# Kernel optimization log

Hardware: AMD Instinct MI355X
Metric: run time of the kernel (lower is better)

## Reference

```python
import jax, jax.numpy as jnp
import numpy as np

N_NODES = 50000
N_EDGES = 800000
IN_FEATS, H_FEATS, N_CLASSES = 64, 64, 16


def setup_inputs() -> dict:
    key = jax.random.key(0)
    ks = jax.random.split(key, 8)
    x = jax.random.normal(ks[0], (N_NODES, IN_FEATS), dtype=jnp.float32)
    src = jax.random.randint(ks[1], (N_EDGES,), 0, N_NODES, dtype=jnp.int64)
    dst = jax.random.randint(ks[2], (N_EDGES,), 0, N_NODES, dtype=jnp.int64)
    W_self1 = jax.random.normal(ks[3], (IN_FEATS, H_FEATS), dtype=jnp.float32) / np.sqrt(IN_FEATS)
    W_neigh1 = jax.random.normal(ks[4], (IN_FEATS, H_FEATS), dtype=jnp.float32) / np.sqrt(IN_FEATS)
    b1 = jnp.zeros((H_FEATS,), dtype=jnp.float32)
    W_self2 = jax.random.normal(ks[5], (H_FEATS, N_CLASSES), dtype=jnp.float32) / np.sqrt(H_FEATS)
    W_neigh2 = jax.random.normal(ks[6], (H_FEATS, N_CLASSES), dtype=jnp.float32) / np.sqrt(H_FEATS)
    b2 = jnp.zeros((N_CLASSES,), dtype=jnp.float32)
    return {"x": x, "src": src, "dst": dst,
            "W_self1": W_self1, "W_neigh1": W_neigh1, "b1": b1,
            "W_self2": W_self2, "W_neigh2": W_neigh2, "b2": b2}


def _mean_agg(h, src, dst, n_nodes):
    # gather source-node features along edges, sum into destinations, divide by in-degree
    summed = jax.ops.segment_sum(h[src], dst, num_segments=n_nodes)  # [N, d]
    deg = jax.ops.segment_sum(jnp.ones_like(src, dtype=h.dtype), dst, num_segments=n_nodes)
    return summed / jnp.maximum(deg, 1.0)[:, None]  # zero in-degree -> zeros (DGL semantics)


def _sage_layer(h, src, dst, W_self, W_neigh, b):
    h_neigh = _mean_agg(h, src, dst, h.shape[0])
    return h @ W_self + h_neigh @ W_neigh + b


def reference(x, src, dst, W_self1, W_neigh1, b1, W_self2, W_neigh2, b2):
    h = _sage_layer(x, src, dst, W_self1, W_neigh1, b1)
    h = jax.nn.relu(h)
    out = _sage_layer(h, src, dst, W_self2, W_neigh2, b2)
    return out
```

## Files before the change

kernel.cpp:

```cpp
#include <hip/hip_runtime.h>
#include <hip/hip_bf16.h>
#include <cstring>


#define FEATS 64
#define CLS   16
#define EPT   16
#define CAP   5120

typedef unsigned short bf16_t;
typedef float floatx2 __attribute__((ext_vector_type(2)));

__device__ __forceinline__ float bfbits2f(unsigned lo16) {
    unsigned v = lo16 << 16;
    float f;
    __builtin_memcpy(&f, &v, 4);
    return f;
}
__device__ __forceinline__ bf16_t f2bf(float f) {
    unsigned u;
    __builtin_memcpy(&u, &f, 4);
    u = (u + 0x7FFFu + ((u >> 16) & 1u)) >> 16;
    return (bf16_t)u;
}
__device__ __forceinline__ unsigned pack2(float a, float b) {
    return (unsigned)f2bf(a) | ((unsigned)f2bf(b) << 16);
}
__device__ __forceinline__ unsigned pack4_fp8(float a, float b, float c, float d) {
    int q = __builtin_amdgcn_cvt_pk_fp8_f32(a, b, 0, false);
    q = __builtin_amdgcn_cvt_pk_fp8_f32(c, d, q, true);
    return (unsigned)q;
}

__global__ __launch_bounds__(256) void fused_pg_kernel(
    const int* __restrict__ src, const int* __restrict__ dst,
    int* __restrict__ bucket_cnt, int* __restrict__ epart, int E,
    const float* __restrict__ x, const float* __restrict__ Ws,
    const float* __restrict__ Wn, bf16_t* __restrict__ selfo,
    unsigned char* __restrict__ t1, int N, int nbp)
{
    __shared__ float smem[16512];
    int t = threadIdx.x;

    if ((int)blockIdx.x < nbp) {
        int* hist = (int*)smem;
        int* base = hist + 256;
        int e0 = blockIdx.x * (256 * EPT);
        hist[t] = 0;
        __syncthreads();
        int pk[EPT];
        int bk[EPT];
#pragma unroll
        for (int j = 0; j < EPT; ++j) {
            int e = e0 + j * 256 + t;
            if (e < E) {
                int d = dst[e];
                pk[j] = (src[e] << 8) | (d & 255);
                bk[j] = d >> 8;
                atomicAdd(&hist[bk[j]], 1);
            } else bk[j] = -1;
        }
        __syncthreads();
        int c = hist[t];
        if (c) base[t] = atomicAdd(&bucket_cnt[t], c);
        hist[t] = 0;
        __syncthreads();
#pragma unroll
        for (int j = 0; j < EPT; ++j) {
            if (bk[j] >= 0) {
                int r = atomicAdd(&hist[bk[j]], 1);
                epart[bk[j] * CAP + base[bk[j]] + r] = pk[j];
            }
        }
        return;
    }

    float* Wc = smem;
    float* xs = smem + 8192;
    int node0 = ((int)blockIdx.x - nbp) * 128;

    for (int idx = t; idx < 64 * 128; idx += 256) {
        int k = idx >> 7, c = idx & 127;
        Wc[idx] = (c < 64) ? Ws[k * 64 + c] : Wn[k * 64 + (c - 64)];
    }
    for (int idx = t; idx < 128 * 16; idx += 256) {
        int row = idx >> 4, c4 = idx & 15;
        int node = node0 + row;
        float4 v = (node < N) ? ((const float4*)(x + (size_t)node * 64))[c4]
                              : make_float4(0.f, 0.f, 0.f, 0.f);
        float* p = &xs[row * 65 + c4 * 4];
        p[0] = v.x; p[1] = v.y; p[2] = v.z; p[3] = v.w;
    }
    __syncthreads();

    int m = t & 31;
    int g = t >> 5;
    float acc[4][16];
#pragma unroll
    for (int j = 0; j < 4; ++j)
#pragma unroll
        for (int c = 0; c < 16; ++c) acc[j][c] = 0.f;

    for (int k = 0; k < 64; ++k) {
        float w[16];
        const float* wp = &Wc[k * 128 + g * 16];
#pragma unroll
        for (int c = 0; c < 16; ++c) w[c] = wp[c];
        float a0 = xs[m * 65 + k];
        float a1 = xs[(m + 32) * 65 + k];
        float a2 = xs[(m + 64) * 65 + k];
        float a3 = xs[(m + 96) * 65 + k];
#pragma unroll
        for (int c = 0; c < 16; ++c) {
            acc[0][c] += a0 * w[c];
            acc[1][c] += a1 * w[c];
            acc[2][c] += a2 * w[c];
            acc[3][c] += a3 * w[c];
        }
    }
#pragma unroll
    for (int j = 0; j < 4; ++j) {
        int node = node0 + m + 32 * j;
        if (node < N) {
            if (g < 4) {
                bf16_t* dstp = selfo + (size_t)node * 64 + g * 16;
                uint4 p0, p1;
                p0.x = pack2(acc[j][0],  acc[j][1]);  p0.y = pack2(acc[j][2],  acc[j][3]);
                p0.z = pack2(acc[j][4],  acc[j][5]);  p0.w = pack2(acc[j][6],  acc[j][7]);
                p1.x = pack2(acc[j][8],  acc[j][9]);  p1.y = pack2(acc[j][10], acc[j][11]);
                p1.z = pack2(acc[j][12], acc[j][13]); p1.w = pack2(acc[j][14], acc[j][15]);
                *(uint4*)(dstp) = p0;
                *(uint4*)(dstp + 8) = p1;
            } else {
                unsigned char* dstp = t1 + (size_t)node * 64 + (g - 4) * 16;
                uint4 q;
                q.x = pack4_fp8(acc[j][0],  acc[j][1],  acc[j][2],  acc[j][3]);
                q.y = pack4_fp8(acc[j][4],  acc[j][5],  acc[j][6],  acc[j][7]);
                q.z = pack4_fp8(acc[j][8],  acc[j][9],  acc[j][10], acc[j][11]);
                q.w = pack4_fp8(acc[j][12], acc[j][13], acc[j][14], acc[j][15]);
                *(uint4*)(dstp) = q;
            }
        }
    }
}

__global__ __launch_bounds__(256) void buildcsr_kernel(const int* __restrict__ epart,
                                                       const int* __restrict__ bucket_cnt,
                                                       int* __restrict__ row_start,
                                                       unsigned short* __restrict__ deg16,
                                                       int* __restrict__ csr, int N) {
    __shared__ int cnt[256];
    __shared__ int pref[256];
    __shared__ int s[256];
    int t = threadIdx.x;
    int b = blockIdx.x;
    int ebeg = b * CAP;
    int ecnt = bucket_cnt[b];
    cnt[t] = 0;
    __syncthreads();
    for (int e = t; e < ecnt; e += 256)
        atomicAdd(&cnt[epart[ebeg + e] & 255], 1);
    __syncthreads();
    int v = cnt[t];
    s[t] = v;
    __syncthreads();
    for (int off = 1; off < 256; off <<= 1) {
        int u = (t >= off) ? s[t - off] : 0;
        __syncthreads();
        s[t] += u;
        __syncthreads();
    }
    pref[t] = s[t] - v;
    int node = b * 256 + t;
    if (node < N) {
        row_start[node] = ebeg + pref[t];
        deg16[node] = (unsigned short)v;
    }
    cnt[t] = 0;
    __syncthreads();
    for (int e = t; e < ecnt; e += 256) {
        int pk = epart[ebeg + e];
        int ln = pk & 255;
        int r = atomicAdd(&cnt[ln], 1);
        csr[ebeg + pref[ln] + r] = pk >> 8;
    }
}

__global__ __launch_bounds__(256) void gather64_kernel(
    const int* __restrict__ csr, const int* __restrict__ row_start,
    const unsigned short* __restrict__ deg16,
    const unsigned char* __restrict__ t1, const bf16_t* __restrict__ selfo,
    bf16_t* __restrict__ h1, const float* __restrict__ b1, int N)
{
    int wid = (blockIdx.x * 256 + threadIdx.x) >> 6;
    int lane = threadIdx.x & 63;
    int eslot = lane >> 4;
    int cg = lane & 15;
    if (wid >= N) return;
    int beg = row_start[wid];
    int d = deg16[wid];
    float ax = 0.f, ay = 0.f, az = 0.f, aw = 0.f;
    int i = eslot;
    for (; i + 12 < d; i += 16) {
        int s0 = csr[beg + i];
        int s1 = csr[beg + i + 4];
        int s2 = csr[beg + i + 8];
        int s3 = csr[beg + i + 12];
        unsigned r0 = *(const unsigned*)(t1 + (size_t)s0 * 64 + cg * 4);
        unsigned r1 = *(const unsigned*)(t1 + (size_t)s1 * 64 + cg * 4);
        unsigned r2 = *(const unsigned*)(t1 + (size_t)s2 * 64 + cg * 4);
        unsigned r3 = *(const unsigned*)(t1 + (size_t)s3 * 64 + cg * 4);
        floatx2 p0 = __builtin_amdgcn_cvt_pk_f32_fp8((int)r0, false);
        floatx2 q0 = __builtin_amdgcn_cvt_pk_f32_fp8((int)r0, true);
        floatx2 p1 = __builtin_amdgcn_cvt_pk_f32_fp8((int)r1, false);
        floatx2 q1 = __builtin_amdgcn_cvt_pk_f32_fp8((int)r1, true);
        floatx2 p2 = __builtin_amdgcn_cvt_pk_f32_fp8((int)r2, false);
        floatx2 q2 = __builtin_amdgcn_cvt_pk_f32_fp8((int)r2, true);
        floatx2 p3 = __builtin_amdgcn_cvt_pk_f32_fp8((int)r3, false);
        floatx2 q3 = __builtin_amdgcn_cvt_pk_f32_fp8((int)r3, true);
        ax += p0.x + p1.x + p2.x + p3.x;
        ay += p0.y + p1.y + p2.y + p3.y;
        az += q0.x + q1.x + q2.x + q3.x;
        aw += q0.y + q1.y + q2.y + q3.y;
    }
    for (; i < d; i += 4) {
        int s0 = csr[beg + i];
        unsigned r0 = *(const unsigned*)(t1 + (size_t)s0 * 64 + cg * 4);
        floatx2 p0 = __builtin_amdgcn_cvt_pk_f32_fp8((int)r0, false);
        floatx2 q0 = __builtin_amdgcn_cvt_pk_f32_fp8((int)r0, true);
        ax += p0.x; ay += p0.y; az += q0.x; aw += q0.y;
    }
    ax += __shfl_xor(ax, 16); ay += __shfl_xor(ay, 16);
    az += __shfl_xor(az, 16); aw += __shfl_xor(aw, 16);
    ax += __shfl_xor(ax, 32); ay += __shfl_xor(ay, 32);
    az += __shfl_xor(az, 32); aw += __shfl_xor(aw, 32);
    if (eslot == 0) {
        float inv = 1.f / fmaxf((float)d, 1.f);
        size_t o = (size_t)wid * 64 + cg * 4;
        uint2 su = *(const uint2*)(selfo + o);
        float4 bb = *(const float4*)(b1 + cg * 4);
        float rx = fmaxf(bfbits2f(su.x & 0xffff) + ax * inv + bb.x, 0.f);
        float ry = fmaxf(bfbits2f(su.x >> 16)    + ay * inv + bb.y, 0.f);
        float rz = fmaxf(bfbits2f(su.y & 0xffff) + az * inv + bb.z, 0.f);
        float rw = fmaxf(bfbits2f(su.y >> 16)    + aw * inv + bb.w, 0.f);
        uint2 pk;
        pk.x = pack2(rx, ry);
        pk.y = pack2(rz, rw);
        *(uint2*)(h1 + o) = pk;
    }
}

__global__ __launch_bounds__(256) void gemm2_kernel(
    const bf16_t* __restrict__ h1, const float* __restrict__ Ws,
    const float* __restrict__ Wn, float* __restrict__ outp,
    bf16_t* __restrict__ t2, int N)
{
    __shared__ float Wc[64 * 32];
    __shared__ float xs[128 * 65];
    int t = threadIdx.x;
    int node0 = blockIdx.x * 128;

    for (int idx = t; idx < 64 * 32; idx += 256) {
        int k = idx >> 5, c = idx & 31;
        Wc[idx] = (c < 16) ? Ws[k * 16 + c] : Wn[k * 16 + (c - 16)];
    }
    for (int idx = t; idx < 128 * 8; idx += 256) {
        int row = idx >> 3, c8 = idx & 7;
        int node = node0 + row;
        float* p = &xs[row * 65 + c8 * 8];
        if (node < N) {
            uint4 u = *(const uint4*)(h1 + (size_t)node * 64 + c8 * 8);
            p[0] = bfbits2f(u.x & 0xffff); p[1] = bfbits2f(u.x >> 16);
            p[2] = bfbits2f(u.y & 0xffff); p[3] = bfbits2f(u.y >> 16);
            p[4] = bfbits2f(u.z & 0xffff); p[5] = bfbits2f(u.z >> 16);
            p[6] = bfbits2f(u.w & 0xffff); p[7] = bfbits2f(u.w >> 16);
        } else {
            for (int qq = 0; qq < 8; ++qq) p[qq] = 0.f;
        }
    }
    __syncthreads();

    int m = t & 31;
    int g = t >> 5;
    float acc[4][4];
#pragma unroll
    for (int j = 0; j < 4; ++j)
#pragma unroll
        for (int c = 0; c < 4; ++c) acc[j][c] = 0.f;

    for (int k = 0; k < 64; ++k) {
        float w[4];
        const float* wp = &Wc[k * 32 + g * 4];
#pragma unroll
        for (int c = 0; c < 4; ++c) w[c] = wp[c];
        float a0 = xs[m * 65 + k];
        float a1 = xs[(m + 32) * 65 + k];
        float a2 = xs[(m + 64) * 65 + k];
        float a3 = xs[(m + 96) * 65 + k];
#pragma unroll
        for (int c = 0; c < 4; ++c) {
            acc[0][c] += a0 * w[c];
            acc[1][c] += a1 * w[c];
            acc[2][c] += a2 * w[c];
            acc[3][c] += a3 * w[c];
        }
    }
#pragma unroll
    for (int j = 0; j < 4; ++j) {
        int node = node0 + m + 32 * j;
        if (node < N) {
            if (g < 4) {
                *(float4*)(outp + (size_t)node * 16 + g * 4) =
                    make_float4(acc[j][0], acc[j][1], acc[j][2], acc[j][3]);
            } else {
                uint2 pk;
                pk.x = pack2(acc[j][0], acc[j][1]);
                pk.y = pack2(acc[j][2], acc[j][3]);
                *(uint2*)(t2 + (size_t)node * 16 + (g - 4) * 4) = pk;
            }
        }
    }
}

__global__ __launch_bounds__(256) void gather16_kernel(
    const int* __restrict__ csr, const int* __restrict__ row_start,
    const unsigned short* __restrict__ deg16,
    const bf16_t* __restrict__ t2,
    float* __restrict__ outp, const float* __restrict__ b2, int N)
{
    int gt = blockIdx.x * 256 + threadIdx.x;
    int node = gt >> 3;
    int c2 = gt & 7;
    if (node >= N) return;
    int beg = row_start[node];
    int d = deg16[node];
    int end = beg + d;
    float a0 = 0.f, a1 = 0.f;
    int i = beg;
    for (; i + 4 <= end; i += 4) {
        int s0 = csr[i], s1 = csr[i + 1], s2 = csr[i + 2], s3 = csr[i + 3];
        unsigned u0 = *(const unsigned*)(t2 + (size_t)s0 * 16 + c2 * 2);
        unsigned u1 = *(const unsigned*)(t2 + (size_t)s1 * 16 + c2 * 2);
        unsigned u2 = *(const unsigned*)(t2 + (size_t)s2 * 16 + c2 * 2);
        unsigned u3 = *(const unsigned*)(t2 + (size_t)s3 * 16 + c2 * 2);
        a0 += bfbits2f(u0 & 0xffff) + bfbits2f(u1 & 0xffff)
            + bfbits2f(u2 & 0xffff) + bfbits2f(u3 & 0xffff);
        a1 += bfbits2f(u0 >> 16) + bfbits2f(u1 >> 16)
            + bfbits2f(u2 >> 16) + bfbits2f(u3 >> 16);
    }
    for (; i < end; ++i) {
        int s = csr[i];
        unsigned u = *(const unsigned*)(t2 + (size_t)s * 16 + c2 * 2);
        a0 += bfbits2f(u & 0xffff);
        a1 += bfbits2f(u >> 16);
    }
    float inv = 1.f / fmaxf((float)d, 1.f);
    size_t o = (size_t)node * 16 + c2 * 2;
    outp[o]     += a0 * inv + b2[c2 * 2];
    outp[o + 1] += a1 * inv + b2[c2 * 2 + 1];
}

extern "C" void kernel_launch(void* const* d_in, const int* in_sizes, int n_in,
                              void* d_out, int out_size, void* d_ws, size_t ws_size,
                              hipStream_t stream) {
    const float* x   = (const float*)d_in[0];
    const int*   src = (const int*)d_in[1];
    const int*   dst = (const int*)d_in[2];
    const float* Ws1 = (const float*)d_in[3];
    const float* Wn1 = (const float*)d_in[4];
    const float* b1  = (const float*)d_in[5];
    const float* Ws2 = (const float*)d_in[6];
    const float* Wn2 = (const float*)d_in[7];
    const float* b2  = (const float*)d_in[8];
    float* outp = (float*)d_out;

    const int N = in_sizes[0] / FEATS;
    const int E = in_sizes[1];
    const int B = (N + 255) / 256;
    const int NBP = (E + 256 * EPT - 1) / (256 * EPT);
    const int NBG = (N + 127) / 128;

    char* p = (char*)d_ws;
    auto align16 = [](char* q) { return (char*)(((size_t)q + 15) & ~(size_t)15); };
    int* bucket_cnt    = (int*)p;                  p = (char*)(bucket_cnt + 256);
    int* epart         = (int*)p;                  p = (char*)(epart + (size_t)B * CAP);
    int* csr           = (int*)p;                  p = (char*)(csr + (size_t)B * CAP);
    int* row_start     = (int*)align16(p);         p = (char*)(row_start + N);
    unsigned short* deg16 = (unsigned short*)align16(p); p = (char*)(deg16 + N);
    bf16_t* selfo      = (bf16_t*)align16(p);      p = (char*)(selfo + (size_t)N * 64);
    unsigned char* t1  = (unsigned char*)align16(p); p = (char*)(t1 + (size_t)N * 64);
    bf16_t* h1         = (bf16_t*)align16(p);      p = (char*)(h1 + (size_t)N * 64);
    bf16_t* t2         = (bf16_t*)align16(p);

    hipMemsetAsync(bucket_cnt, 0, 256 * sizeof(int), stream);

    fused_pg_kernel<<<NBP + NBG, 256, 0, stream>>>(
        src, dst, bucket_cnt, epart, E, x, Ws1, Wn1, selfo, t1, N, NBP);
    buildcsr_kernel<<<B, 256, 0, stream>>>(epart, bucket_cnt, row_start, deg16, csr, N);

    gather64_kernel<<<((size_t)N * 64 + 255) / 256, 256, 0, stream>>>(
        csr, row_start, deg16, t1, selfo, h1, b1, N);
    gemm2_kernel<<<(N + 127) / 128, 256, 0, stream>>>(h1, Ws2, Wn2, outp, t2, N);
    gather16_kernel<<<((size_t)N * 8 + 255) / 256, 256, 0, stream>>>(
        csr, row_start, deg16, t2, outp, b2, N);
}
```

Measured before the change: 161.0 us.

## Rebalance gather lane mapping, use wavefront-per-node layer-2 gather, widen CSR build blocks

The layer-1 gather now gives each lane 8 fp8 features (8-byte loads) with 8 edge slots per wavefront instead of 4-byte loads across 4 slots. The layer-2 gather moves from 8 threads per node walking all edges serially to one wavefront per node, with 16 edge slots reduced by shuffles and a single float4 read-modify-write of the output. The CSR build kernel runs with 512 threads so the edge-count and scatter loops take half as many iterations. The cost is more shuffle reductions and more idle lanes on low-degree nodes, since average degree is about 16.

```diff
diff --git a/kernel.cpp b/kernel.cpp
--- a/kernel.cpp
+++ b/kernel.cpp
@@ -144,7 +144,7 @@
     }
 }
 
-__global__ __launch_bounds__(256) void buildcsr_kernel(const int* __restrict__ epart,
+__global__ __launch_bounds__(512) void buildcsr_kernel(const int* __restrict__ epart,
                                                        const int* __restrict__ bucket_cnt,
                                                        int* __restrict__ row_start,
                                                        unsigned short* __restrict__ deg16,
@@ -156,29 +156,31 @@
     int b = blockIdx.x;
     int ebeg = b * CAP;
     int ecnt = bucket_cnt[b];
-    cnt[t] = 0;
-    __syncthreads();
-    for (int e = t; e < ecnt; e += 256)
+    if (t < 256) cnt[t] = 0;
+    __syncthreads();
+    for (int e = t; e < ecnt; e += 512)
         atomicAdd(&cnt[epart[ebeg + e] & 255], 1);
     __syncthreads();
-    int v = cnt[t];
-    s[t] = v;
+    int v = 0;
+    if (t < 256) { v = cnt[t]; s[t] = v; }
     __syncthreads();
     for (int off = 1; off < 256; off <<= 1) {
-        int u = (t >= off) ? s[t - off] : 0;
+        int u = (t < 256 && t >= off) ? s[t - off] : 0;
         __syncthreads();
-        s[t] += u;
+        if (t < 256) s[t] += u;
         __syncthreads();
     }
-    pref[t] = s[t] - v;
-    int node = b * 256 + t;
-    if (node < N) {
-        row_start[node] = ebeg + pref[t];
-        deg16[node] = (unsigned short)v;
-    }
-    cnt[t] = 0;
-    __syncthreads();
-    for (int e = t; e < ecnt; e += 256) {
+    if (t < 256) {
+        pref[t] = s[t] - v;
+        int node = b * 256 + t;
+        if (node < N) {
+            row_start[node] = ebeg + pref[t];
+            deg16[node] = (unsigned short)v;
+        }
+        cnt[t] = 0;
+    }
+    __syncthreads();
+    for (int e = t; e < ecnt; e += 512) {
         int pk = epart[ebeg + e];
         int ln = pk & 255;
         int r = atomicAdd(&cnt[ln], 1);
@@ -194,59 +196,69 @@
 {
     int wid = (blockIdx.x * 256 + threadIdx.x) >> 6;
     int lane = threadIdx.x & 63;
-    int eslot = lane >> 4;
-    int cg = lane & 15;
+    int eslot = lane >> 3;
+    int cg = lane & 7;
     if (wid >= N) return;
     int beg = row_start[wid];
     int d = deg16[wid];
-    float ax = 0.f, ay = 0.f, az = 0.f, aw = 0.f;
+    float a[8];
+#pragma unroll
+    for (int c = 0; c < 8; ++c) a[c] = 0.f;
     int i = eslot;
-    for (; i + 12 < d; i += 16) {
+    for (; i + 8 < d; i += 16) {
         int s0 = csr[beg + i];
-        int s1 = csr[beg + i + 4];
-        int s2 = csr[beg + i + 8];
-        int s3 = csr[beg + i + 12];
-        unsigned r0 = *(const unsigned*)(t1 + (size_t)s0 * 64 + cg * 4);
-        unsigned r1 = *(const unsigned*)(t1 + (size_t)s1 * 64 + cg * 4);
-        unsigned r2 = *(const unsigned*)(t1 + (size_t)s2 * 64 + cg * 4);
-        unsigned r3 = *(const unsigned*)(t1 + (size_t)s3 * 64 + cg * 4);
-        floatx2 p0 = __builtin_amdgcn_cvt_pk_f32_fp8((int)r0, false);
-        floatx2 q0 = __builtin_amdgcn_cvt_pk_f32_fp8((int)r0, true);
-        floatx2 p1 = __builtin_amdgcn_cvt_pk_f32_fp8((int)r1, false);
-        floatx2 q1 = __builtin_amdgcn_cvt_pk_f32_fp8((int)r1, true);
-        floatx2 p2 = __builtin_amdgcn_cvt_pk_f32_fp8((int)r2, false);
-        floatx2 q2 = __builtin_amdgcn_cvt_pk_f32_fp8((int)r2, true);
-        floatx2 p3 = __builtin_amdgcn_cvt_pk_f32_fp8((int)r3, false);
-        floatx2 q3 = __builtin_amdgcn_cvt_pk_f32_fp8((int)r3, true);
-        ax += p0.x + p1.x + p2.x + p3.x;
-        ay += p0.y + p1.y + p2.y + p3.y;
-        az += q0.x + q1.x + q2.x + q3.x;
-        aw += q0.y + q1.y + q2.y + q3.y;
-    }
-    for (; i < d; i += 4) {
+        int s1 = csr[beg + i + 8];
+        uint2 r0 = *(const uint2*)(t1 + (size_t)s0 * 64 + cg * 8);
+        uint2 r1 = *(const uint2*)(t1 + (size_t)s1 * 64 + cg * 8);
+        floatx2 p0 = __builtin_amdgcn_cvt_pk_f32_fp8((int)r0.x, false);
+        floatx2 p1 = __builtin_amdgcn_cvt_pk_f32_fp8((int)r0.x, true);
+        floatx2 p2 = __builtin_amdgcn_cvt_pk_f32_fp8((int)r0.y, false);
+        floatx2 p3 = __builtin_amdgcn_cvt_pk_f32_fp8((int)r0.y, true);
+        floatx2 q0 = __builtin_amdgcn_cvt_pk_f32_fp8((int)r1.x, false);
+        floatx2 q1 = __builtin_amdgcn_cvt_pk_f32_fp8((int)r1.x, true);
+        floatx2 q2 = __builtin_amdgcn_cvt_pk_f32_fp8((int)r1.y, false);
+        floatx2 q3 = __builtin_amdgcn_cvt_pk_f32_fp8((int)r1.y, true);
+        a[0] += p0.x + q0.x;  a[1] += p0.y + q0.y;
+        a[2] += p1.x + q1.x;  a[3] += p1.y + q1.y;
+        a[4] += p2.x + q2.x;  a[5] += p2.y + q2.y;
+        a[6] += p3.x + q3.x;  a[7] += p3.y + q3.y;
+    }
+    if (i < d) {
         int s0 = csr[beg + i];
-        unsigned r0 = *(const unsigned*)(t1 + (size_t)s0 * 64 + cg * 4);
-        floatx2 p0 = __builtin_amdgcn_cvt_pk_f32_fp8((int)r0, false);
-        floatx2 q0 = __builtin_amdgcn_cvt_pk_f32_fp8((int)r0, true);
-        ax += p0.x; ay += p0.y; az += q0.x; aw += q0.y;
-    }
-    ax += __shfl_xor(ax, 16); ay += __shfl_xor(ay, 16);
-    az += __shfl_xor(az, 16); aw += __shfl_xor(aw, 16);
-    ax += __shfl_xor(ax, 32); ay += __shfl_xor(ay, 32);
-    az += __shfl_xor(az, 32); aw += __shfl_xor(aw, 32);
+        uint2 r0 = *(const uint2*)(t1 + (size_t)s0 * 64 + cg * 8);
+        floatx2 p0 = __builtin_amdgcn_cvt_pk_f32_fp8((int)r0.x, false);
+        floatx2 p1 = __builtin_amdgcn_cvt_pk_f32_fp8((int)r0.x, true);
+        floatx2 p2 = __builtin_amdgcn_cvt_pk_f32_fp8((int)r0.y, false);
+        floatx2 p3 = __builtin_amdgcn_cvt_pk_f32_fp8((int)r0.y, true);
+        a[0] += p0.x; a[1] += p0.y; a[2] += p1.x; a[3] += p1.y;
+        a[4] += p2.x; a[5] += p2.y; a[6] += p3.x; a[7] += p3.y;
+    }
+#pragma unroll
+    for (int c = 0; c < 8; ++c) {
+        a[c] += __shfl_xor(a[c], 8);
+        a[c] += __shfl_xor(a[c], 16);
+        a[c] += __shfl_xor(a[c], 32);
+    }
     if (eslot == 0) {
         float inv = 1.f / fmaxf((float)d, 1.f);
-        size_t o = (size_t)wid * 64 + cg * 4;
-        uint2 su = *(const uint2*)(selfo + o);
-        float4 bb = *(const float4*)(b1 + cg * 4);
-        float rx = fmaxf(bfbits2f(su.x & 0xffff) + ax * inv + bb.x, 0.f);
-        float ry = fmaxf(bfbits2f(su.x >> 16)    + ay * inv + bb.y, 0.f);
-        float rz = fmaxf(bfbits2f(su.y & 0xffff) + az * inv + bb.z, 0.f);
-        float rw = fmaxf(bfbits2f(su.y >> 16)    + aw * inv + bb.w, 0.f);
-        uint2 pk;
-        pk.x = pack2(rx, ry);
-        pk.y = pack2(rz, rw);
-        *(uint2*)(h1 + o) = pk;
+        size_t o = (size_t)wid * 64 + cg * 8;
+        uint4 su = *(const uint4*)(selfo + o);
+        float4 b0 = *(const float4*)(b1 + cg * 8);
+        float4 b4 = *(const float4*)(b1 + cg * 8 + 4);
+        float r0 = fmaxf(bfbits2f(su.x & 0xffff) + a[0] * inv + b0.x, 0.f);
+        float r1 = fmaxf(bfbits2f(su.x >> 16)    + a[1] * inv + b0.y, 0.f);
+        float r2 = fmaxf(bfbits2f(su.y & 0xffff) + a[2] * inv + b0.z, 0.f);
+        float r3 = fmaxf(bfbits2f(su.y >> 16)    + a[3] * inv + b0.w, 0.f);
+        float r4 = fmaxf(bfbits2f(su.z & 0xffff) + a[4] * inv + b4.x, 0.f);
+        float r5 = fmaxf(bfbits2f(su.z >> 16)    + a[5] * inv + b4.y, 0.f);
+        float r6 = fmaxf(bfbits2f(su.w & 0xffff) + a[6] * inv + b4.z, 0.f);
+        float r7 = fmaxf(bfbits2f(su.w >> 16)    + a[7] * inv + b4.w, 0.f);
+        uint4 pk;
+        pk.x = pack2(r0, r1);
+        pk.y = pack2(r2, r3);
+        pk.z = pack2(r4, r5);
+        pk.w = pack2(r6, r7);
+        *(uint4*)(h1 + o) = pk;
     }
 }
 
@@ -328,36 +340,41 @@
     const bf16_t* __restrict__ t2,
     float* __restrict__ outp, const float* __restrict__ b2, int N)
 {
-    int gt = blockIdx.x * 256 + threadIdx.x;
-    int node = gt >> 3;
-    int c2 = gt & 7;
-    if (node >= N) return;
-    int beg = row_start[node];
-    int d = deg16[node];
-    int end = beg + d;
-    float a0 = 0.f, a1 = 0.f;
-    int i = beg;
-    for (; i + 4 <= end; i += 4) {
-        int s0 = csr[i], s1 = csr[i + 1], s2 = csr[i + 2], s3 = csr[i + 3];
-        unsigned u0 = *(const unsigned*)(t2 + (size_t)s0 * 16 + c2 * 2);
-        unsigned u1 = *(const unsigned*)(t2 + (size_t)s1 * 16 + c2 * 2);
-        unsigned u2 = *(const unsigned*)(t2 + (size_t)s2 * 16 + c2 * 2);
-        unsigned u3 = *(const unsigned*)(t2 + (size_t)s3 * 16 + c2 * 2);
-        a0 += bfbits2f(u0 & 0xffff) + bfbits2f(u1 & 0xffff)
-            + bfbits2f(u2 & 0xffff) + bfbits2f(u3 & 0xffff);
-        a1 += bfbits2f(u0 >> 16) + bfbits2f(u1 >> 16)
-            + bfbits2f(u2 >> 16) + bfbits2f(u3 >> 16);
-    }
-    for (; i < end; ++i) {
-        int s = csr[i];
-        unsigned u = *(const unsigned*)(t2 + (size_t)s * 16 + c2 * 2);
-        a0 += bfbits2f(u & 0xffff);
-        a1 += bfbits2f(u >> 16);
-    }
-    float inv = 1.f / fmaxf((float)d, 1.f);
-    size_t o = (size_t)node * 16 + c2 * 2;
-    outp[o]     += a0 * inv + b2[c2 * 2];
-    outp[o + 1] += a1 * inv + b2[c2 * 2 + 1];
+    int wid = (blockIdx.x * 256 + threadIdx.x) >> 6;
+    int lane = threadIdx.x & 63;
+    int eslot = lane >> 2;
+    int cg = lane & 3;
+    if (wid >= N) return;
+    int beg = row_start[wid];
+    int d = deg16[wid];
+    float a0 = 0.f, a1 = 0.f, a2 = 0.f, a3 = 0.f;
+    for (int i = eslot; i < d; i += 16) {
+        int s0 = csr[beg + i];
+        uint2 u = *(const uint2*)(t2 + (size_t)s0 * 16 + cg * 4);
+        a0 += bfbits2f(u.x & 0xffff);
+        a1 += bfbits2f(u.x >> 16);
+        a2 += bfbits2f(u.y & 0xffff);
+        a3 += bfbits2f(u.y >> 16);
+    }
+    a0 += __shfl_xor(a0, 4); a1 += __shfl_xor(a1, 4);
+    a2 += __shfl_xor(a2, 4); a3 += __shfl_xor(a3, 4);
+    a0 += __shfl_xor(a0, 8); a1 += __shfl_xor(a1, 8);
+    a2 += __shfl_xor(a2, 8); a3 += __shfl_xor(a3, 8);
+    a0 += __shfl_xor(a0, 16); a1 += __shfl_xor(a1, 16);
+    a2 += __shfl_xor(a2, 16); a3 += __shfl_xor(a3, 16);
+    a0 += __shfl_xor(a0, 32); a1 += __shfl_xor(a1, 32);
+    a2 += __shfl_xor(a2, 32); a3 += __shfl_xor(a3, 32);
+    if (eslot == 0) {
+        float inv = 1.f / fmaxf((float)d, 1.f);
+        size_t o = (size_t)wid * 16 + cg * 4;
+        float4 bb = *(const float4*)(b2 + cg * 4);
+        float4 ov = *(const float4*)(outp + o);
+        ov.x += a0 * inv + bb.x;
+        ov.y += a1 * inv + bb.y;
+        ov.z += a2 * inv + bb.z;
+        ov.w += a3 * inv + bb.w;
+        *(float4*)(outp + o) = ov;
+    }
 }
 
 extern "C" void kernel_launch(void* const* d_in, const int* in_sizes, int n_in,
@@ -396,11 +413,11 @@
 
     fused_pg_kernel<<<NBP + NBG, 256, 0, stream>>>(
         src, dst, bucket_cnt, epart, E, x, Ws1, Wn1, selfo, t1, N, NBP);
-    buildcsr_kernel<<<B, 256, 0, stream>>>(epart, bucket_cnt, row_start, deg16, csr, N);
+    buildcsr_kernel<<<B, 512, 0, stream>>>(epart, bucket_cnt, row_start, deg16, csr, N);
 
     gather64_kernel<<<((size_t)N * 64 + 255) / 256, 256, 0, stream>>>(
         csr, row_start, deg16, t1, selfo, h1, b1, N);
     gemm2_kernel<<<(N + 127) / 128, 256, 0, stream>>>(h1, Ws2, Wn2, outp, t2, N);
-    gather16_kernel<<<((size_t)N * 8 + 255) / 256, 256, 0, stream>>>(
+    gather16_kernel<<<((size_t)N * 64 + 255) / 256, 256, 0, stream>>>(
         csr, row_start, deg16, t2, outp, b2, N);
 }
```

New measurement: 162.2 us. No clear change (+0.8%).
